# Kernel tuning notes

Hardware: AMD Instinct MI355X
Metric: run time of the kernel (lower is better)

## Reference

```python
import jax, jax.numpy as jnp
import numpy as np

NUM_CLASSES = 19
RADIUS = 2  # hardcoded in the original forward
B, H, W = 2, 1024, 2048

# Math note: the original computes, per class k, dist = edt(onehot_pad) + edt(1-onehot_pad)
# (scipy edt = distance to nearest zero). At every pixel exactly one term is nonzero, and it
# equals the Euclidean distance to the nearest opposite-valued pixel WITHIN the zero-padded
# array. Then dist[dist > 2] = 0 and edgemap = (sum_k dist_k) > 0. Hence a pixel is an edge
# pixel iff for some class k its Euclidean-disk(2) neighborhood (inside the padded array;
# out-of-bounds pixels never count) contains BOTH a 1 and a 0 of onehot_k. The disk of radius
# 2 is exactly the 13 integer offsets with dx^2+dy^2 <= 4, so we implement this with one
# small convolution counting ones in the disk (c) and comparing against the number of
# in-bounds disk pixels (nb): edge_k = (c > 0) & (c < nb).

def _disk_kernel():
    r = jnp.arange(-RADIUS, RADIUS + 1)
    d2 = r[:, None] ** 2 + r[None, :] ** 2
    return (d2 <= RADIUS ** 2).astype(jnp.float32)[None, None]  # (1,1,5,5), 13 ones


def setup_inputs() -> dict:
    key = jax.random.key(0)
    gtmasks = jax.random.randint(key, (B, 1, H, W), 0, 20, dtype=jnp.int32)
    return {"gtmasks": gtmasks}


def reference(gtmasks) -> jnp.ndarray:
    b, _, h, w = gtmasks.shape
    lab = gtmasks[:, 0].astype(jnp.int32)  # (B,H,W) integer class labels
    classes = jnp.arange(1, NUM_CLASSES + 1, dtype=jnp.int32)
    # one-hot for classes 1..19, padded with a ring of zeros (np.pad constant 0)
    oh = (lab[:, None, :, :] == classes[None, :, None, None]).astype(jnp.float32)  # (B,K,H,W)
    oh = jnp.pad(oh, ((0, 0), (0, 0), (1, 1), (1, 1)))  # (B,K,H+2,W+2)

    k = _disk_kernel()
    x = oh.reshape(b * NUM_CLASSES, 1, h + 2, w + 2)
    pad = [(RADIUS, RADIUS), (RADIUS, RADIUS)]
    c = jax.lax.conv_general_dilated(x, k, (1, 1), pad)  # ones-count in disk, OOB -> 0
    ones = jnp.ones((1, 1, h + 2, w + 2), jnp.float32)
    nb = jax.lax.conv_general_dilated(ones, k, (1, 1), pad)  # in-bounds disk size

    edge_k = (c > 0) & (c < nb)  # disk contains both a 1 and an in-bounds 0
    edge_k = edge_k.reshape(b, NUM_CLASSES, h + 2, w + 2)[:, :, 1:-1, 1:-1]  # crop pad ring
    edge = jnp.any(edge_k, axis=1, keepdims=True)  # (B,1,H,W)
    return edge.astype(jnp.int32)
```

## Files before the change

kernel.cpp:

```cpp
#include <hip/hip_runtime.h>
#include <stdint.h>

namespace {
constexpr int kH = 1024;
constexpr int kW = 2048;
constexpr int kNBX = kW / 256;
}

typedef int v4i __attribute__((ext_vector_type(4)));

__device__ __forceinline__ uint32_t pk2(int lo, int hi) {
    return (uint32_t)lo | ((uint32_t)hi << 16);
}
__device__ __forceinline__ uint32_t pkmin(uint32_t a, uint32_t b) {
    uint32_t d;
    asm("v_pk_min_i16 %0, %1, %2" : "=v"(d) : "v"(a), "v"(b));
    return d;
}
__device__ __forceinline__ uint32_t pkmax(uint32_t a, uint32_t b) {
    uint32_t d;
    asm("v_pk_max_i16 %0, %1, %2" : "=v"(d) : "v"(a), "v"(b));
    return d;
}
__device__ __forceinline__ uint32_t algn(uint32_t hi, uint32_t lo) {
    return (lo >> 16) | (hi << 16);
}

__global__ __launch_bounds__(256) void boundary_edge_kernel(const int* __restrict__ lab,
                                                            int* __restrict__ out) {
    const int lane = threadIdx.x;
    const int bx = blockIdx.x;
    const int x0 = (bx * 64 + lane) * 4;
    const int y0 = (blockIdx.y * 4 + threadIdx.y) * 4;
    const int bi = blockIdx.z;
    const int* img = lab + (size_t)bi * kH * kW;

    const bool hasL = (bx > 0);
    const bool hasR = (bx < kNBX - 1);

    uint32_t hv = 0;
    {
        const int j = lane & 7;
        const int ry = min(max(y0 + j - 2, 0), kH - 1);
        const bool doL = (lane < 8) && hasL;
        const bool doR = (lane >= 8) && (lane < 16) && hasR;
        if (doL | doR) {
            const int xh = (lane < 8) ? (bx * 256 - 2) : (bx * 256 + 256);
            const int2 t = *reinterpret_cast<const int2*>(img + (size_t)ry * kW + xh);
            hv = pk2(t.x, t.y);
        }
    }

    uint32_t r0a[8], r0b[8];
    uint32_t r1mn01[8], r1mx01[8], r1mn23[8], r1mx23[8];
    uint32_t r2mn01[8], r2mx01[8], r2mn23[8], r2mx23[8];

#pragma unroll
    for (int j = 0; j < 8; ++j) {
        const int ry = min(max(y0 + j - 2, 0), kH - 1);
        const int4 v = *reinterpret_cast<const int4*>(img + (size_t)ry * kW + x0);
        const uint32_t A = pk2(v.x, v.y);
        const uint32_t B = pk2(v.z, v.w);
        r0a[j] = A;
        r0b[j] = B;
        if (j >= 1 && j <= 6) {
            uint32_t Bl = __shfl_up(B, 1);
            uint32_t Ar = __shfl_down(A, 1);
            const uint32_t fL = hasL ? __shfl(hv, j)     : pk2(v.x, v.x);
            const uint32_t fR = hasR ? __shfl(hv, j + 8) : pk2(v.w, v.w);
            if (lane == 0)  Bl = fL;
            if (lane == 63) Ar = fR;

            const uint32_t L1 = algn(A, Bl);
            const uint32_t M  = algn(B, A);
            const uint32_t N  = algn(Ar, B);

            r1mn01[j] = pkmin(pkmin(L1, A), M);
            r1mx01[j] = pkmax(pkmax(L1, A), M);
            r1mn23[j] = pkmin(pkmin(M, B), N);
            r1mx23[j] = pkmax(pkmax(M, B), N);
            if (j >= 2 && j <= 5) {
                r2mn01[j] = pkmin(r1mn01[j], pkmin(Bl, B));
                r2mx01[j] = pkmax(r1mx01[j], pkmax(Bl, B));
                r2mn23[j] = pkmin(r1mn23[j], pkmin(A, Ar));
                r2mx23[j] = pkmax(r1mx23[j], pkmax(A, Ar));
            }
        }
    }

    bool xb[4];
#pragma unroll
    for (int i = 0; i < 4; ++i) {
        const int x = x0 + i;
        xb[i] = (x <= 1) | (x >= kW - 2);
    }

#pragma unroll
    for (int k = 0; k < 4; ++k) {
        const uint32_t mn01 = pkmin(pkmin(r2mn01[k + 2], pkmin(r1mn01[k + 1], r1mn01[k + 3])),
                                    pkmin(r0a[k], r0a[k + 4]));
        const uint32_t mx01 = pkmax(pkmax(r2mx01[k + 2], pkmax(r1mx01[k + 1], r1mx01[k + 3])),
                                    pkmax(r0a[k], r0a[k + 4]));
        const uint32_t mn23 = pkmin(pkmin(r2mn23[k + 2], pkmin(r1mn23[k + 1], r1mn23[k + 3])),
                                    pkmin(r0b[k], r0b[k + 4]));
        const uint32_t mx23 = pkmax(pkmax(r2mx23[k + 2], pkmax(r1mx23[k + 1], r1mx23[k + 3])),
                                    pkmax(r0b[k], r0b[k + 4]));

        const int y = y0 + k;
        const bool yb = (y <= 1) | (y >= kH - 2);

        const uint32_t d01 = mn01 ^ mx01;
        const uint32_t d23 = mn23 ^ mx23;

        v4i r;
        r.x = ((mx01 & 0xFFFFu) != 0u && (((d01 & 0xFFFFu) != 0u) | yb | xb[0])) ? 1 : 0;
        r.y = ((mx01 >> 16)     != 0u && (((d01 >> 16)     != 0u) | yb | xb[1])) ? 1 : 0;
        r.z = ((mx23 & 0xFFFFu) != 0u && (((d23 & 0xFFFFu) != 0u) | yb | xb[2])) ? 1 : 0;
        r.w = ((mx23 >> 16)     != 0u && (((d23 >> 16)     != 0u) | yb | xb[3])) ? 1 : 0;

        __builtin_nontemporal_store(r,
            reinterpret_cast<v4i*>(out + ((size_t)(bi * kH + y) * kW + x0)));
    }
}

extern "C" void kernel_launch(void* const* d_in, const int* in_sizes, int n_in,
                              void* d_out, int out_size, void* d_ws, size_t ws_size,
                              hipStream_t stream) {
    const int* lab = (const int*)d_in[0];
    int* out = (int*)d_out;
    dim3 block(64, 4, 1);
    dim3 grid(kW / 256, kH / 16, 2);
    boundary_edge_kernel<<<grid, block, 0, stream>>>(lab, out);
}
```

Baseline: 10.52 us.

## Stage block tile rows in LDS via async global_load_lds to share halo rows

Each 256-thread block now loads its 20-row by 256-column tile (16 rows plus 2-row halos) into shared memory using direct global-to-LDS loads, plus small left and right column halos. Waves then read their 8 overlapping rows from LDS, so the same rows are not re-fetched from global memory by neighbouring waves. Horizontal neighbours come from LDS reads instead of cross-lane shuffles. This cuts redundant global traffic (from 8 row reads per 4 output rows down to 20 per 16) but adds a block-wide barrier, LDS traffic, and possible bank conflicts from the 264-int row stride.

```diff
diff --git a/kernel.cpp b/kernel.cpp
--- a/kernel.cpp
+++ b/kernel.cpp
@@ -4,10 +4,9 @@
 namespace {
 constexpr int kH = 1024;
 constexpr int kW = 2048;
-constexpr int kNBX = kW / 256;
+constexpr int kRows = 20;
+constexpr int kStride = 264;
 }
-
-typedef int v4i __attribute__((ext_vector_type(4)));
 
 __device__ __forceinline__ uint32_t pk2(int lo, int hi) {
     return (uint32_t)lo | ((uint32_t)hi << 16);
@@ -26,30 +25,47 @@
     return (lo >> 16) | (hi << 16);
 }
 
+typedef int v4i __attribute__((ext_vector_type(4)));
+
 __global__ __launch_bounds__(256) void boundary_edge_kernel(const int* __restrict__ lab,
                                                             int* __restrict__ out) {
+    __shared__ int ctr[kRows][kStride];
+    __shared__ int hL[kRows][2];
+    __shared__ int hR[kRows][2];
+
     const int lane = threadIdx.x;
-    const int bx = blockIdx.x;
-    const int x0 = (bx * 64 + lane) * 4;
-    const int y0 = (blockIdx.y * 4 + threadIdx.y) * 4;
-    const int bi = blockIdx.z;
+    const int ty   = threadIdx.y;
+    const int bx0  = blockIdx.x * 256;
+    const int by0  = blockIdx.y * 16;
+    const int bi   = blockIdx.z;
     const int* img = lab + (size_t)bi * kH * kW;
 
-    const bool hasL = (bx > 0);
-    const bool hasR = (bx < kNBX - 1);
-
-    uint32_t hv = 0;
-    {
-        const int j = lane & 7;
-        const int ry = min(max(y0 + j - 2, 0), kH - 1);
-        const bool doL = (lane < 8) && hasL;
-        const bool doR = (lane >= 8) && (lane < 16) && hasR;
-        if (doL | doR) {
-            const int xh = (lane < 8) ? (bx * 256 - 2) : (bx * 256 + 256);
-            const int2 t = *reinterpret_cast<const int2*>(img + (size_t)ry * kW + xh);
-            hv = pk2(t.x, t.y);
+#pragma unroll
+    for (int rr = 0; rr < 5; ++rr) {
+        const int r  = ty * 5 + rr;
+        const int ry = min(max(by0 + r - 2, 0), kH - 1);
+        const int* src = img + (size_t)ry * kW + bx0 + lane * 4;
+        __builtin_amdgcn_global_load_lds(
+            (const __attribute__((address_space(1))) void*)src,
+            (__attribute__((address_space(3))) void*)&ctr[r][0],
+            16, 0, 0);
+    }
+    if (ty == 0) {
+        if (lane < kRows) {
+            const int r  = lane;
+            const int ry = min(max(by0 + r - 2, 0), kH - 1);
+            const size_t ro = (size_t)ry * kW;
+            hL[r][0] = img[ro + max(bx0 - 2, 0)];
+            hL[r][1] = img[ro + max(bx0 - 1, 0)];
+        } else if (lane >= 32 && lane < 32 + kRows) {
+            const int r  = lane - 32;
+            const int ry = min(max(by0 + r - 2, 0), kH - 1);
+            const size_t ro = (size_t)ry * kW;
+            hR[r][0] = img[ro + min(bx0 + 256, kW - 1)];
+            hR[r][1] = img[ro + min(bx0 + 257, kW - 1)];
         }
     }
+    __syncthreads();
 
     uint32_t r0a[8], r0b[8];
     uint32_t r1mn01[8], r1mx01[8], r1mn23[8], r1mx23[8];
@@ -57,19 +73,22 @@
 
 #pragma unroll
     for (int j = 0; j < 8; ++j) {
-        const int ry = min(max(y0 + j - 2, 0), kH - 1);
-        const int4 v = *reinterpret_cast<const int4*>(img + (size_t)ry * kW + x0);
+        const int r = ty * 4 + j;
+        const int* cp = &ctr[r][lane * 4];
+        const int4 v = *reinterpret_cast<const int4*>(cp);
         const uint32_t A = pk2(v.x, v.y);
         const uint32_t B = pk2(v.z, v.w);
         r0a[j] = A;
         r0b[j] = B;
         if (j >= 1 && j <= 6) {
-            uint32_t Bl = __shfl_up(B, 1);
-            uint32_t Ar = __shfl_down(A, 1);
-            const uint32_t fL = hasL ? __shfl(hv, j)     : pk2(v.x, v.x);
-            const uint32_t fR = hasR ? __shfl(hv, j + 8) : pk2(v.w, v.w);
-            if (lane == 0)  Bl = fL;
-            if (lane == 63) Ar = fR;
+            const int2* lp = (lane == 0)  ? reinterpret_cast<const int2*>(&hL[r][0])
+                                          : reinterpret_cast<const int2*>(cp - 2);
+            const int2* rp = (lane == 63) ? reinterpret_cast<const int2*>(&hR[r][0])
+                                          : reinterpret_cast<const int2*>(cp + 4);
+            const int2 Lp = *lp;
+            const int2 Rp = *rp;
+            const uint32_t Bl = pk2(Lp.x, Lp.y);
+            const uint32_t Ar = pk2(Rp.x, Rp.y);
 
             const uint32_t L1 = algn(A, Bl);
             const uint32_t M  = algn(B, A);
@@ -91,7 +110,7 @@
     bool xb[4];
 #pragma unroll
     for (int i = 0; i < 4; ++i) {
-        const int x = x0 + i;
+        const int x = bx0 + lane * 4 + i;
         xb[i] = (x <= 1) | (x >= kW - 2);
     }
 
@@ -106,7 +125,7 @@
         const uint32_t mx23 = pkmax(pkmax(r2mx23[k + 2], pkmax(r1mx23[k + 1], r1mx23[k + 3])),
                                     pkmax(r0b[k], r0b[k + 4]));
 
-        const int y = y0 + k;
+        const int y = by0 + ty * 4 + k;
         const bool yb = (y <= 1) | (y >= kH - 2);
 
         const uint32_t d01 = mn01 ^ mx01;
@@ -119,7 +138,7 @@
         r.w = ((mx23 >> 16)     != 0u && (((d23 >> 16)     != 0u) | yb | xb[3])) ? 1 : 0;
 
         __builtin_nontemporal_store(r,
-            reinterpret_cast<v4i*>(out + ((size_t)(bi * kH + y) * kW + x0)));
+            reinterpret_cast<v4i*>(out + ((size_t)(bi * kH + y) * kW + bx0 + lane * 4)));
     }
 }
 
```

After: 10.47 us. No clear change (-0.5%).
